# Performance work log

Measured on AMD Instinct MI355X. Metric: run time of the kernel, lower is better.

Reference implementation:

```python
import jax, jax.numpy as jnp
import numpy as np

TOP_K = 2
LOGIT_SCALE = 1.0


def setup_inputs() -> dict:
    key = jax.random.key(0)
    k = jax.random.split(key, 5)
    B, S, C = 1, 1024, 1024
    E, I = 8, 1024           # experts, per-expert intermediate
    x = jax.random.normal(k[0], (B, S, C), dtype=jnp.float32)
    router_w = jax.random.normal(k[1], (E, C), dtype=jnp.float32) * 0.02
    w_in = jax.random.normal(k[2], (E, 2 * I, C), dtype=jnp.float32) * 0.02
    b_in = jnp.zeros((E, 2 * I), dtype=jnp.float32)
    w_out = jax.random.normal(k[3], (E, C, I), dtype=jnp.float32) * 0.02
    b_out = jnp.zeros((E, C), dtype=jnp.float32)
    return {"x": x, "router_w": router_w, "w_in": w_in, "b_in": b_in,
            "w_out": w_out, "b_out": b_out}


def reference(x, router_w, w_in, b_in, w_out, b_out):
    B, S, C = x.shape
    E = router_w.shape[0]
    xt = x.reshape(-1, C)                               # [T, C] flattened tokens
    T = xt.shape[0]

    # Router: softmax over all experts, then top-k probs as combine weights.
    logits = (xt @ router_w.T) * LOGIT_SCALE            # [T, E]
    probs = jax.nn.softmax(logits, axis=-1)
    top_w, top_idx = jax.lax.top_k(probs, TOP_K)        # [T, K]

    # Sparse gate matrix: nonzero only at the top-k experts per token.
    gate = jnp.zeros((T, E), dtype=probs.dtype)
    gate = gate.at[jnp.arange(T)[:, None], top_idx].set(top_w)  # [T, E]

    # Expert SwiGLU MLP, dense over experts, masked combine by gate.
    h = jnp.einsum('tc,eoc->teo', xt, w_in) + b_in      # [T, E, 2I]
    g, u = jnp.split(h, 2, axis=-1)                     # gate / input halves
    a = jax.nn.silu(g) * u                              # swiglu  [T, E, I]
    y = jnp.einsum('tei,eci->tec', a, w_out) + b_out    # [T, E, C]
    out = jnp.einsum('te,tec->tc', gate, y)             # combine top-k experts
    return out.reshape(B, S, C)
```

## Files before the change

kernel.cpp:

```cpp
#include <hip/hip_runtime.h>
#include <hip/hip_bf16.h>
#include <stdint.h>

#define TTOK 1024
#define CDIM 1024
#define NEXP 8
#define IDIM 1024
#define TWOI 2048
#define NSLOT 2048

typedef float f32x4 __attribute__((ext_vector_type(4)));
typedef short s16x8 __attribute__((ext_vector_type(8)));
typedef unsigned short u16;
typedef u16 u16x4 __attribute__((ext_vector_type(4)));
typedef u16 u16x8 __attribute__((ext_vector_type(8)));

__device__ __forceinline__ u16 f2bf(float f) {
  unsigned x = __float_as_uint(f);
  x += 0x7fffu + ((x >> 16) & 1u);
  return (u16)(x >> 16);
}

__device__ __forceinline__ void gload_lds16(const void* g, void* l) {
  __builtin_amdgcn_global_load_lds(
      (const __attribute__((address_space(1))) void*)g,
      (__attribute__((address_space(3))) void*)l, 16, 0, 0);
}

__global__ __launch_bounds__(64) void router_k(const float* __restrict__ x,
                                               const float* __restrict__ rw,
                                               float* __restrict__ topw,
                                               int* __restrict__ topidx,
                                               u16* __restrict__ xb) {
  const int t = blockIdx.x;
  const int lane = threadIdx.x;
  float p[NEXP];
#pragma unroll
  for (int e = 0; e < NEXP; ++e) p[e] = 0.f;
  const float* xr = x + (size_t)t * CDIM;
  u16* xbr = xb + (size_t)t * CDIM;
  for (int c0 = lane * 4; c0 < CDIM; c0 += 64 * 4) {
    f32x4 xv = *(const f32x4*)(xr + c0);
    u16x4 xc;
#pragma unroll
    for (int q = 0; q < 4; ++q) xc[q] = f2bf(xv[q]);
    *(u16x4*)(xbr + c0) = xc;
#pragma unroll
    for (int e = 0; e < NEXP; ++e) {
      f32x4 wv = *(const f32x4*)(rw + (size_t)e * CDIM + c0);
      p[e] += xv[0] * wv[0] + xv[1] * wv[1] + xv[2] * wv[2] + xv[3] * wv[3];
    }
  }
#pragma unroll
  for (int e = 0; e < NEXP; ++e) {
    float v = p[e];
#pragma unroll
    for (int off = 32; off >= 1; off >>= 1) v += __shfl_xor(v, off);
    p[e] = v;
  }
  if (lane == 0) {
    float m = p[0];
#pragma unroll
    for (int e = 1; e < NEXP; ++e) m = fmaxf(m, p[e]);
    float pe[NEXP];
    float den = 0.f;
#pragma unroll
    for (int e = 0; e < NEXP; ++e) { pe[e] = __expf(p[e] - m); den += pe[e]; }
    int i0 = 0;
#pragma unroll
    for (int e = 1; e < NEXP; ++e) if (p[e] > p[i0]) i0 = e;
    int i1 = (i0 == 0) ? 1 : 0;
#pragma unroll
    for (int e = 0; e < NEXP; ++e) if (e != i0 && p[e] > p[i1]) i1 = e;
    const float inv = 1.f / den;
    topw[t * 2] = pe[i0] * inv;
    topw[t * 2 + 1] = pe[i1] * inv;
    topidx[t * 2] = i0;
    topidx[t * 2 + 1] = i1;
  }
}

__global__ __launch_bounds__(1024) void build_k(const int* __restrict__ topidx,
                                                int* __restrict__ meta,
                                                int* __restrict__ slot_token,
                                                int* __restrict__ slot_expert,
                                                int* __restrict__ tok2slot) {
  __shared__ int cnt[NEXP], off[NEXP], cur[NEXP];
  const int t = threadIdx.x;
  if (t < NEXP) { cnt[t] = 0; cur[t] = 0; }
  __syncthreads();
  const int e0 = topidx[t * 2];
  const int e1 = topidx[t * 2 + 1];
  atomicAdd(&cnt[e0], 1);
  atomicAdd(&cnt[e1], 1);
  __syncthreads();
  if (t == 0) {
    int acc = 0;
    for (int e = 0; e < NEXP; ++e) { off[e] = acc; acc += cnt[e]; }
  }
  __syncthreads();
  if (t < NEXP) { meta[t] = cnt[t]; meta[16 + t] = off[t]; }
  {
    const int p0 = atomicAdd(&cur[e0], 1);
    const int s0 = off[e0] + p0;
    slot_token[s0] = t;
    slot_expert[s0] = e0;
    tok2slot[t * 2] = s0;
    const int p1 = atomicAdd(&cur[e1], 1);
    const int s1 = off[e1] + p1;
    slot_token[s1] = t;
    slot_expert[s1] = e1;
    tok2slot[t * 2 + 1] = s1;
  }
}

template <int BM, bool GATHER, bool BIAS>
__global__ __launch_bounds__(256) void gemm_k(const u16* __restrict__ A,
                                              const float* __restrict__ W,
                                              float* __restrict__ O,
                                              const float* __restrict__ bias,
                                              const int* __restrict__ meta,
                                              const int* __restrict__ slot_token,
                                              int N, int K) {
  constexpr int BN = 64;
  constexpr int WM = BM / 2;
  constexpr int WN = BN / 2;
  constexpr int MR = WM / 16;
  constexpr int NR = WN / 16;

  const int e = blockIdx.z;
  const int cnt = meta[e];
  const int m0 = blockIdx.y * BM;
  if (m0 >= cnt) return;
  const int off = meta[16 + e];
  const int n0 = blockIdx.x * BN;

  __shared__ u16 sA[BM * 64];
  __shared__ u16 sB[BN * 64];

  const int tid = threadIdx.x;
  const int lane = tid & 63;
  const int w = tid >> 6;
  const int wr = w >> 1;
  const int wc = w & 1;

  const u16* aSrc[BM / 32];
#pragma unroll
  for (int i = 0; i < BM / 32; ++i) {
    const int r = w * (BM / 4) + i * 8 + (lane >> 3);
    int rr = m0 + r;
    if (rr > cnt - 1) rr = cnt - 1;
    const int rowg = GATHER ? slot_token[off + rr] : (off + rr);
    const int cs = (lane & 7) ^ (r & 7);
    aSrc[i] = A + (size_t)rowg * K + cs * 8;
  }

  const int brow = tid >> 2;
  const int bq = tid & 3;
  const float* bSrc = W + ((size_t)e * N + (n0 + brow)) * K + bq * 16;
  u16* sBrow = sB + brow * 64;
  const int brow7 = brow & 7;

  f32x4 acc[MR][NR];
#pragma unroll
  for (int m = 0; m < MR; ++m)
#pragma unroll
    for (int n = 0; n < NR; ++n) acc[m][n] = (f32x4){0.f, 0.f, 0.f, 0.f};

  for (int k0 = 0; k0 < K; k0 += 64) {
#pragma unroll
    for (int i = 0; i < BM / 32; ++i)
      gload_lds16(aSrc[i] + k0, sA + (w * (BM / 4) + i * 8) * 64 + lane * 8);

    {
      const float* bs = bSrc + k0;
      f32x4 v0 = *(const f32x4*)(bs);
      f32x4 v1 = *(const f32x4*)(bs + 4);
      f32x4 v2 = *(const f32x4*)(bs + 8);
      f32x4 v3 = *(const f32x4*)(bs + 12);
      u16x8 lo, hi;
#pragma unroll
      for (int q = 0; q < 4; ++q) lo[q] = f2bf(v0[q]);
#pragma unroll
      for (int q = 0; q < 4; ++q) lo[4 + q] = f2bf(v1[q]);
#pragma unroll
      for (int q = 0; q < 4; ++q) hi[q] = f2bf(v2[q]);
#pragma unroll
      for (int q = 0; q < 4; ++q) hi[4 + q] = f2bf(v3[q]);
      *(u16x8*)(sBrow + (((bq * 2) ^ brow7) * 8)) = lo;
      *(u16x8*)(sBrow + (((bq * 2 + 1) ^ brow7) * 8)) = hi;
    }
    __syncthreads();

#pragma unroll
    for (int kh = 0; kh < 2; ++kh) {
      const int j = kh * 4 + (lane >> 4);
      s16x8 af[MR], bf[NR];
#pragma unroll
      for (int m = 0; m < MR; ++m) {
        const int r = wr * WM + m * 16 + (lane & 15);
        af[m] = *(const s16x8*)(sA + r * 64 + ((j ^ (r & 7)) * 8));
      }
#pragma unroll
      for (int n = 0; n < NR; ++n) {
        const int r = wc * WN + n * 16 + (lane & 15);
        bf[n] = *(const s16x8*)(sB + r * 64 + ((j ^ (r & 7)) * 8));
      }
#pragma unroll
      for (int m = 0; m < MR; ++m)
#pragma unroll
        for (int n = 0; n < NR; ++n)
          acc[m][n] = __builtin_amdgcn_mfma_f32_16x16x32_bf16(af[m], bf[n], acc[m][n], 0, 0, 0);
    }
    __syncthreads();
  }

#pragma unroll
  for (int m = 0; m < MR; ++m) {
#pragma unroll
    for (int jj = 0; jj < 4; ++jj) {
      const int tr = wr * WM + m * 16 + ((lane >> 4) * 4) + jj;
      if (m0 + tr < cnt) {
        const size_t slot = (size_t)(off + m0 + tr);
#pragma unroll
        for (int n = 0; n < NR; ++n) {
          const int col = n0 + wc * WN + n * 16 + (lane & 15);
          float v = acc[m][n][jj];
          if (BIAS) v += bias[(size_t)e * N + col];
          O[slot * N + col] = v;
        }
      }
    }
  }
}

__global__ __launch_bounds__(256) void swiglu_k(const float* __restrict__ h,
                                                const float* __restrict__ b_in,
                                                const int* __restrict__ slot_expert,
                                                u16* __restrict__ a) {
  const int s = blockIdx.x;
  const int e = slot_expert[s];
  const int i = threadIdx.x * 4;
  f32x4 g = *(const f32x4*)(h + (size_t)s * TWOI + i);
  f32x4 u = *(const f32x4*)(h + (size_t)s * TWOI + IDIM + i);
  f32x4 bg = *(const f32x4*)(b_in + (size_t)e * TWOI + i);
  f32x4 bu = *(const f32x4*)(b_in + (size_t)e * TWOI + IDIM + i);
  u16x4 o;
#pragma unroll
  for (int q = 0; q < 4; ++q) {
    const float gg = g[q] + bg[q];
    const float uu = u[q] + bu[q];
    const float sv = gg / (1.f + __expf(-gg));
    o[q] = f2bf(sv * uu);
  }
  *(u16x4*)(a + (size_t)s * IDIM + i) = o;
}

__global__ __launch_bounds__(256) void combine_k(const float* __restrict__ y,
                                                 const float* __restrict__ topw,
                                                 const int* __restrict__ tok2slot,
                                                 float* __restrict__ out) {
  const int idx = blockIdx.x * 256 + threadIdx.x;
  const int t = idx >> 8;
  const int c4 = (idx & 255) * 4;
  const int s0 = tok2slot[t * 2];
  const int s1 = tok2slot[t * 2 + 1];
  const float w0 = topw[t * 2];
  const float w1 = topw[t * 2 + 1];
  f32x4 y0 = *(const f32x4*)(y + (size_t)s0 * CDIM + c4);
  f32x4 y1 = *(const f32x4*)(y + (size_t)s1 * CDIM + c4);
  f32x4 o;
#pragma unroll
  for (int q = 0; q < 4; ++q) o[q] = w0 * y0[q] + w1 * y1[q];
  *(f32x4*)(out + (size_t)t * CDIM + c4) = o;
}

extern "C" void kernel_launch(void* const* d_in, const int* in_sizes, int n_in,
                              void* d_out, int out_size, void* d_ws, size_t ws_size,
                              hipStream_t stream) {
  const float* x = (const float*)d_in[0];
  const float* rw = (const float*)d_in[1];
  const float* w_in = (const float*)d_in[2];
  const float* b_in = (const float*)d_in[3];
  const float* w_out = (const float*)d_in[4];
  const float* b_out = (const float*)d_in[5];
  float* out = (float*)d_out;
  char* ws = (char*)d_ws;

  int* meta = (int*)ws;
  int* slot_token = (int*)(ws + 1024);
  int* slot_expert = (int*)(ws + 1024 + 8192);
  int* tok2slot = (int*)(ws + 1024 + 16384);
  float* topw = (float*)(ws + 1024 + 24576);
  int* topidx = (int*)(ws + 1024 + 32768);
  u16* xb = (u16*)(ws + 65536);
  float* h = (float*)(ws + 65536 + (2u << 20));
  u16* a = (u16*)(ws + 65536 + (18u << 20));
  float* y = (float*)(ws + 65536 + (22u << 20));

  router_k<<<TTOK, 64, 0, stream>>>(x, rw, topw, topidx, xb);
  build_k<<<1, 1024, 0, stream>>>(topidx, meta, slot_token, slot_expert, tok2slot);
  gemm_k<128, true, false><<<dim3(32, 16, NEXP), 256, 0, stream>>>(
      xb, w_in, h, nullptr, meta, slot_token, TWOI, CDIM);
  swiglu_k<<<NSLOT, 256, 0, stream>>>(h, b_in, slot_expert, a);
  gemm_k<64, false, true><<<dim3(16, 32, NEXP), 256, 0, stream>>>(
      a, w_out, y, b_out, meta, slot_token, CDIM, IDIM);
  combine_k<<<1024, 256, 0, stream>>>(y, topw, tok2slot, out);
}
```

Before: 219.1 us.

## Double-buffer LDS tiles in expert GEMM to overlap loads with MFMA

Splits the A and B shared-memory tiles into two buffers. The next K-tile is prefetched while MFMAs run on the current one: A goes through direct global-to-LDS loads, and B is loaded into registers, converted to bf16 and stored after the compute. This removes one barrier per iteration and hides global load latency behind math. It doubles LDS use and raises register pressure from holding the prefetched B values, which may lower occupancy.

```diff
diff --git a/kernel.cpp b/kernel.cpp
--- a/kernel.cpp
+++ b/kernel.cpp
@@ -127,6 +127,7 @@
   constexpr int WN = BN / 2;
   constexpr int MR = WM / 16;
   constexpr int NR = WN / 16;
+  constexpr int AG = BM / 32;
 
   const int e = blockIdx.z;
   const int cnt = meta[e];
@@ -135,8 +136,8 @@
   const int off = meta[16 + e];
   const int n0 = blockIdx.x * BN;
 
-  __shared__ u16 sA[BM * 64];
-  __shared__ u16 sB[BN * 64];
+  __shared__ u16 sA[2][BM * 64];
+  __shared__ u16 sB[2][BN * 64];
 
   const int tid = threadIdx.x;
   const int lane = tid & 63;
@@ -144,9 +145,9 @@
   const int wr = w >> 1;
   const int wc = w & 1;
 
-  const u16* aSrc[BM / 32];
-#pragma unroll
-  for (int i = 0; i < BM / 32; ++i) {
+  const u16* aSrc[AG];
+#pragma unroll
+  for (int i = 0; i < AG; ++i) {
     const int r = w * (BM / 4) + i * 8 + (lane >> 3);
     int rr = m0 + r;
     if (rr > cnt - 1) rr = cnt - 1;
@@ -154,12 +155,16 @@
     const int cs = (lane & 7) ^ (r & 7);
     aSrc[i] = A + (size_t)rowg * K + cs * 8;
   }
+  int aDst[AG];
+#pragma unroll
+  for (int i = 0; i < AG; ++i) aDst[i] = (w * (BM / 4) + i * 8) * 64 + lane * 8;
 
   const int brow = tid >> 2;
   const int bq = tid & 3;
   const float* bSrc = W + ((size_t)e * N + (n0 + brow)) * K + bq * 16;
-  u16* sBrow = sB + brow * 64;
   const int brow7 = brow & 7;
+  const int bOff0 = brow * 64 + (((bq * 2) ^ brow7) * 8);
+  const int bOff1 = brow * 64 + (((bq * 2 + 1) ^ brow7) * 8);
 
   f32x4 acc[MR][NR];
 #pragma unroll
@@ -167,30 +172,42 @@
 #pragma unroll
     for (int n = 0; n < NR; ++n) acc[m][n] = (f32x4){0.f, 0.f, 0.f, 0.f};
 
+  {
+#pragma unroll
+    for (int i = 0; i < AG; ++i) gload_lds16(aSrc[i], &sA[0][aDst[i]]);
+    f32x4 v0 = *(const f32x4*)(bSrc);
+    f32x4 v1 = *(const f32x4*)(bSrc + 4);
+    f32x4 v2 = *(const f32x4*)(bSrc + 8);
+    f32x4 v3 = *(const f32x4*)(bSrc + 12);
+    u16x8 lo, hi;
+#pragma unroll
+    for (int q = 0; q < 4; ++q) lo[q] = f2bf(v0[q]);
+#pragma unroll
+    for (int q = 0; q < 4; ++q) lo[4 + q] = f2bf(v1[q]);
+#pragma unroll
+    for (int q = 0; q < 4; ++q) hi[q] = f2bf(v2[q]);
+#pragma unroll
+    for (int q = 0; q < 4; ++q) hi[4 + q] = f2bf(v3[q]);
+    *(u16x8*)(&sB[0][bOff0]) = lo;
+    *(u16x8*)(&sB[0][bOff1]) = hi;
+  }
+  __syncthreads();
+
+  int c = 0;
   for (int k0 = 0; k0 < K; k0 += 64) {
-#pragma unroll
-    for (int i = 0; i < BM / 32; ++i)
-      gload_lds16(aSrc[i] + k0, sA + (w * (BM / 4) + i * 8) * 64 + lane * 8);
-
-    {
-      const float* bs = bSrc + k0;
-      f32x4 v0 = *(const f32x4*)(bs);
-      f32x4 v1 = *(const f32x4*)(bs + 4);
-      f32x4 v2 = *(const f32x4*)(bs + 8);
-      f32x4 v3 = *(const f32x4*)(bs + 12);
-      u16x8 lo, hi;
-#pragma unroll
-      for (int q = 0; q < 4; ++q) lo[q] = f2bf(v0[q]);
-#pragma unroll
-      for (int q = 0; q < 4; ++q) lo[4 + q] = f2bf(v1[q]);
-#pragma unroll
-      for (int q = 0; q < 4; ++q) hi[q] = f2bf(v2[q]);
-#pragma unroll
-      for (int q = 0; q < 4; ++q) hi[4 + q] = f2bf(v3[q]);
-      *(u16x8*)(sBrow + (((bq * 2) ^ brow7) * 8)) = lo;
-      *(u16x8*)(sBrow + (((bq * 2 + 1) ^ brow7) * 8)) = hi;
-    }
-    __syncthreads();
+    const int nk = k0 + 64;
+    const bool has_next = nk < K;
+
+    f32x4 v0, v1, v2, v3;
+    if (has_next) {
+#pragma unroll
+      for (int i = 0; i < AG; ++i) gload_lds16(aSrc[i] + nk, &sA[1 - c][aDst[i]]);
+      const float* bs = bSrc + nk;
+      v0 = *(const f32x4*)(bs);
+      v1 = *(const f32x4*)(bs + 4);
+      v2 = *(const f32x4*)(bs + 8);
+      v3 = *(const f32x4*)(bs + 12);
+    }
 
 #pragma unroll
     for (int kh = 0; kh < 2; ++kh) {
@@ -199,12 +216,12 @@
 #pragma unroll
       for (int m = 0; m < MR; ++m) {
         const int r = wr * WM + m * 16 + (lane & 15);
-        af[m] = *(const s16x8*)(sA + r * 64 + ((j ^ (r & 7)) * 8));
+        af[m] = *(const s16x8*)(&sA[c][r * 64 + ((j ^ (r & 7)) * 8)]);
       }
 #pragma unroll
       for (int n = 0; n < NR; ++n) {
         const int r = wc * WN + n * 16 + (lane & 15);
-        bf[n] = *(const s16x8*)(sB + r * 64 + ((j ^ (r & 7)) * 8));
+        bf[n] = *(const s16x8*)(&sB[c][r * 64 + ((j ^ (r & 7)) * 8)]);
       }
 #pragma unroll
       for (int m = 0; m < MR; ++m)
@@ -212,7 +229,23 @@
         for (int n = 0; n < NR; ++n)
           acc[m][n] = __builtin_amdgcn_mfma_f32_16x16x32_bf16(af[m], bf[n], acc[m][n], 0, 0, 0);
     }
+
+    if (has_next) {
+      u16x8 lo, hi;
+#pragma unroll
+      for (int q = 0; q < 4; ++q) lo[q] = f2bf(v0[q]);
+#pragma unroll
+      for (int q = 0; q < 4; ++q) lo[4 + q] = f2bf(v1[q]);
+#pragma unroll
+      for (int q = 0; q < 4; ++q) hi[q] = f2bf(v2[q]);
+#pragma unroll
+      for (int q = 0; q < 4; ++q) hi[4 + q] = f2bf(v3[q]);
+      *(u16x8*)(&sB[1 - c][bOff0]) = lo;
+      *(u16x8*)(&sB[1 - c][bOff1]) = hi;
+    }
+
     __syncthreads();
+    c ^= 1;
   }
 
 #pragma unroll
```

Result: faster. 197.9 us (-9.7%).
